# Kernel tuning notes

Hardware: AMD Instinct MI355X
Metric: run time of the kernel (lower is better)

## Reference

```python
import jax, jax.numpy as jnp
import numpy as np

ROUTING_ITERS = 3
EPS = 1e-12


def squash(s):
    # squash over both pose-matrix dims (axis=[-2,-1])
    n2 = jnp.sum(s * s, axis=(-2, -1), keepdims=True)
    n = jnp.sqrt(n2 + EPS)
    return s * (n2 / (1.0 + n2)) / n


def setup_inputs() -> dict:
    key = jax.random.key(0)
    k1, k2, k3 = jax.random.split(key, 3)
    B, I, O = 32, 4096, 32
    input_poses = jax.random.normal(k1, (B, I, 4, 4), dtype=jnp.float32)
    input_activations = jax.random.uniform(k2, (B, I), dtype=jnp.float32)
    # weight: [num_capsules, num_input_caps, 4, 4] (trans_in=trans_out=False for 4x4->4x4)
    w = jax.random.normal(k3, (O, I, 4, 4), dtype=jnp.float32) * 0.05
    return {"input_poses": input_poses, "input_activations": input_activations, "w": w}


def reference(input_poses, input_activations, w):
    # votes: expand_dims(poses,1) @ w, broadcast over output capsules -> [B,O,I,4,4]
    votes = jnp.einsum("bixy,oiyz->boixz", input_poses, w)
    B, O, I = votes.shape[0], votes.shape[1], votes.shape[2]

    # dynamic routing (routing-by-agreement)
    b = jnp.zeros((B, O, I), dtype=votes.dtype)
    s = None
    for it in range(ROUTING_ITERS):
        c = jax.nn.softmax(b, axis=1)  # couple over output capsules
        s = jnp.einsum("boi,boixy->boxy", c, votes)  # weighted sum [B,O,4,4]
        if it < ROUTING_ITERS - 1:
            v = squash(s)
            b = b + jnp.einsum("boixy,boxy->boi", votes, v)

    capsule_poses = squash(s)  # activation == 'squash'
    capsule_activations = jnp.sqrt(jnp.sum(capsule_poses * capsule_poses, axis=(-2, -1)) + EPS)
    return capsule_poses, capsule_activations
```

## Files before the change

### kernel.cpp

```cpp
#include <hip/hip_runtime.h>
#include <math.h>


#define NB 32
#define NI 4096
#define NO 32
#define I_TILE 16
#define NCHUNK (NI / I_TILE)
#define SOFF (NB * NO * 16)
#define EPSF 1e-12f

#define W_OSTR 10
#define W_ISTR (32 * W_OSTR)
#define W_WORDS (I_TILE * W_ISTR)
#define P_WORDS (NB * I_TILE * 8)

typedef _Float16 v2h __attribute__((ext_vector_type(2)));

#if __has_builtin(__builtin_amdgcn_fdot2)
__device__ __forceinline__ float fdot2(v2h a, v2h b, float c) {
    return __builtin_amdgcn_fdot2(a, b, c, false);
}
#else
__device__ __forceinline__ float fdot2(v2h a, v2h b, float c) {
    return fmaf((float)a.x, (float)b.x, fmaf((float)a.y, (float)b.y, c));
}
#endif

__device__ __forceinline__ v2h pk2h(float a, float b) {
    v2h r; r.x = (_Float16)a; r.y = (_Float16)b; return r;
}

__device__ __forceinline__ unsigned ubits(v2h x) {
    return __builtin_bit_cast(unsigned, x);
}

__device__ __forceinline__ v2h bch(unsigned u) {
    return __builtin_bit_cast(v2h, u);
}

__device__ __forceinline__ float dot4(const float4 a, const float4 b) {
    return fmaf(a.x, b.x, fmaf(a.y, b.y, fmaf(a.z, b.z, a.w * b.w)));
}

__device__ __forceinline__ void fma4(float4& s, const float c, const float4 t) {
    s.x = fmaf(c, t.x, s.x);
    s.y = fmaf(c, t.y, s.y);
    s.z = fmaf(c, t.z, s.z);
    s.w = fmaf(c, t.w, s.w);
}

template <int CTRL>
__device__ __forceinline__ float dpp_add(float x) {
    int xi = __builtin_bit_cast(int, x);
    int yi = __builtin_amdgcn_update_dpp(0, xi, CTRL, 0xf, 0xf, false);
    return x + __builtin_bit_cast(float, yi);
}

__device__ __forceinline__ float sum32(float x) {
    x = dpp_add<0xB1>(x);
    x = dpp_add<0x4E>(x);
    x = dpp_add<0x141>(x);
    x = dpp_add<0x140>(x);
#if __has_builtin(__builtin_amdgcn_permlane16_swap)
    typedef unsigned uv2 __attribute__((ext_vector_type(2)));
    const unsigned xi = __builtin_bit_cast(unsigned, x);
    uv2 r = __builtin_amdgcn_permlane16_swap(xi, xi, false, false);
    return __builtin_bit_cast(float, r.x) + __builtin_bit_cast(float, r.y);
#else
    int t = __builtin_amdgcn_ds_swizzle(__builtin_bit_cast(int, x), 0x401F);
    return x + __builtin_bit_cast(float, t);
#endif
}

__global__ __launch_bounds__(1024, 4) void caps_pass_w(
    const float* __restrict__ poses, const float* __restrict__ w,
    const float* __restrict__ v_buf, float* __restrict__ s_part,
    const int pass)
{
    __shared__ unsigned wsw[W_WORDS];
    __shared__ unsigned psw[P_WORDS];
    const int tid   = threadIdx.x;
    const int chunk = blockIdx.x;
    const int ibase = chunk * I_TILE;

    {
        const int o_l = tid >> 5;
        const int rem = tid & 31;
        const int i_l = rem >> 1;
        const int m   = rem & 1;
        const float* g = w + (((size_t)o_l * NI + ibase + i_l) << 4) + (m << 3);
        const float4 A = *(const float4*)g;
        const float4 B = *(const float4*)(g + 4);
        const int base = i_l * W_ISTR + o_l * W_OSTR + (m << 2);
        *(uint2*)&wsw[base]     = make_uint2(ubits(pk2h(A.x, B.x)),
                                             ubits(pk2h(A.y, B.y)));
        *(uint2*)&wsw[base + 2] = make_uint2(ubits(pk2h(A.z, B.z)),
                                             ubits(pk2h(A.w, B.w)));
    }
    {
        const int b_l = tid >> 5;
        const int rem = tid & 31;
        const int i_l = rem >> 1;
        const int x2  = rem & 1;
        const float* g = poses + (((size_t)b_l * NI + ibase + i_l) << 4)
                       + (x2 << 3);
        const float4 A = *(const float4*)g;
        const float4 B = *(const float4*)(g + 4);
        uint4 st;
        st.x = ubits(pk2h(A.x, A.y)); st.y = ubits(pk2h(A.z, A.w));
        st.z = ubits(pk2h(B.x, B.y)); st.w = ubits(pk2h(B.z, B.w));
        *(uint4*)&psw[((b_l * I_TILE + i_l) << 3) + (x2 << 2)] = st;
    }

    const int o    = tid & 31;
    const int bsub = tid >> 5;
    const int bo   = bsub * NO + o;

    float4 vv0 = {0,0,0,0}, vv1 = {0,0,0,0}, vv2 = {0,0,0,0}, vv3 = {0,0,0,0};
    if (pass > 0) {
        const float4* vp = (const float4*)(v_buf + (bo << 4));
        vv0 = vp[0]; vv1 = vp[1]; vv2 = vp[2]; vv3 = vp[3];
    }

    const unsigned* wrow = &wsw[o * W_OSTR];
    const unsigned* prow = &psw[(bsub * I_TILE) << 3];

    __syncthreads();

    float4 s0 = {0,0,0,0}, s1 = {0,0,0,0}, s2 = {0,0,0,0}, s3 = {0,0,0,0};

    #pragma unroll 2
    for (int i = 0; i < I_TILE; ++i) {
        const uint2 wa = *(const uint2*)&wrow[i * W_ISTR + 0];
        const uint2 wb = *(const uint2*)&wrow[i * W_ISTR + 2];
        const uint2 wc = *(const uint2*)&wrow[i * W_ISTR + 4];
        const uint2 wd = *(const uint2*)&wrow[i * W_ISTR + 6];
        const uint4 pa = *(const uint4*)&prow[(i << 3) + 0];
        const uint4 pb = *(const uint4*)&prow[(i << 3) + 4];

        const v2h p00 = bch(pa.x), p01 = bch(pa.y);
        const v2h p10 = bch(pa.z), p11 = bch(pa.w);
        const v2h p20 = bch(pb.x), p21 = bch(pb.y);
        const v2h p30 = bch(pb.z), p31 = bch(pb.w);
        const v2h w00 = bch(wa.x), w01 = bch(wa.y);
        const v2h w02 = bch(wb.x), w03 = bch(wb.y);
        const v2h w10 = bch(wc.x), w11 = bch(wc.y);
        const v2h w12 = bch(wd.x), w13 = bch(wd.y);

        float4 t0, t1, t2, t3;
        t0.x = fdot2(p00, w00, fdot2(p01, w10, 0.0f));
        t0.y = fdot2(p00, w01, fdot2(p01, w11, 0.0f));
        t0.z = fdot2(p00, w02, fdot2(p01, w12, 0.0f));
        t0.w = fdot2(p00, w03, fdot2(p01, w13, 0.0f));
        t1.x = fdot2(p10, w00, fdot2(p11, w10, 0.0f));
        t1.y = fdot2(p10, w01, fdot2(p11, w11, 0.0f));
        t1.z = fdot2(p10, w02, fdot2(p11, w12, 0.0f));
        t1.w = fdot2(p10, w03, fdot2(p11, w13, 0.0f));
        t2.x = fdot2(p20, w00, fdot2(p21, w10, 0.0f));
        t2.y = fdot2(p20, w01, fdot2(p21, w11, 0.0f));
        t2.z = fdot2(p20, w02, fdot2(p21, w12, 0.0f));
        t2.w = fdot2(p20, w03, fdot2(p21, w13, 0.0f));
        t3.x = fdot2(p30, w00, fdot2(p31, w10, 0.0f));
        t3.y = fdot2(p30, w01, fdot2(p31, w11, 0.0f));
        t3.z = fdot2(p30, w02, fdot2(p31, w12, 0.0f));
        t3.w = fdot2(p30, w03, fdot2(p31, w13, 0.0f));

        float cc;
        if (pass == 0) {
            cc = 1.0f / 32.0f;
        } else {
            const float d = dot4(t0,vv0) + dot4(t1,vv1)
                          + dot4(t2,vv2) + dot4(t3,vv3);
            const float e  = __expf(d);
            const float es = sum32(e);
            cc = __fdividef(e, es);
        }
        fma4(s0, cc, t0); fma4(s1, cc, t1);
        fma4(s2, cc, t2); fma4(s3, cc, t3);
    }

    float4* sp = (float4*)s_part;
    sp[(size_t)((chunk << 2) + 0) * (NB * NO) + bo] = s0;
    sp[(size_t)((chunk << 2) + 1) * (NB * NO) + bo] = s1;
    sp[(size_t)((chunk << 2) + 2) * (NB * NO) + bo] = s2;
    sp[(size_t)((chunk << 2) + 3) * (NB * NO) + bo] = s3;
}

__global__ __launch_bounds__(256) void caps_reduce(
    const float* __restrict__ s_part, float* __restrict__ v_buf,
    float* __restrict__ out, const int pass)
{
    const int e  = threadIdx.x & 63;
    const int c4 = threadIdx.x >> 6;
    const int eg = blockIdx.x * 64 + e;
    const int bo   = eg >> 4;
    const int k    = eg & 15;
    const int col  = ((k >> 2) << 12) + (bo << 2) + (k & 3);

    float acc = 0.0f;
    #pragma unroll 8
    for (int j = 0; j < NCHUNK / 4; ++j) {
        const int c = c4 * (NCHUNK / 4) + j;
        acc += s_part[(size_t)c * SOFF + col];
    }
    __shared__ float red[4][64];
    red[c4][e] = acc;
    __syncthreads();

    if (threadIdx.x < 64) {
        const float a = red[0][e] + red[1][e] + red[2][e] + red[3][e];
        float x = a * a;
        #pragma unroll
        for (int msk = 8; msk >= 1; msk >>= 1)
            x += __shfl_xor(x, msk, 16);
        const float n2 = x;
        const float n  = sqrtf(n2 + EPSF);
        const float sc = (n2 / (1.0f + n2)) / n;
        if (pass < 2) {
            const float vold = (pass == 0) ? 0.0f : v_buf[eg];
            v_buf[eg] = fmaf(sc, a, vold);
        } else {
            out[eg] = sc * a;
            if (k == 0)
                out[NB * NO * 16 + bo] = sqrtf(n2 * sc * sc + EPSF);
        }
    }
}

#define FB_CHUNKS 32
#define FB_IPB (NI / FB_CHUNKS)

__device__ __forceinline__ float4 row_mm(const float4 p, const float4 w0,
                                         const float4 w1, const float4 w2,
                                         const float4 w3) {
    float4 r;
    r.x = fmaf(p.x, w0.x, fmaf(p.y, w1.x, fmaf(p.z, w2.x, p.w * w3.x)));
    r.y = fmaf(p.x, w0.y, fmaf(p.y, w1.y, fmaf(p.z, w2.y, p.w * w3.y)));
    r.z = fmaf(p.x, w0.z, fmaf(p.y, w1.z, fmaf(p.z, w2.z, p.w * w3.z)));
    r.w = fmaf(p.x, w0.w, fmaf(p.y, w1.w, fmaf(p.z, w2.w, p.w * w3.w)));
    return r;
}

__global__ __launch_bounds__(256) void caps_pass_fb(
    const float* __restrict__ poses, const float* __restrict__ w,
    const float* __restrict__ v_buf, float* __restrict__ s_buf, const int mode)
{
    const int tid   = threadIdx.x;
    const int b     = blockIdx.y;
    const int chunk = blockIdx.x;
    const int o     = tid & 31;
    const int g     = tid >> 5;

    float4 v0 = {0,0,0,0}, v1 = {0,0,0,0}, v2 = {0,0,0,0}, v3 = {0,0,0,0};
    if (mode != 0) {
        const float4* vp = (const float4*)(v_buf + (((b * NO) + o) << 4));
        v0 = vp[0]; v1 = vp[1]; v2 = vp[2]; v3 = vp[3];
    }
    float4 s0 = {0,0,0,0}, s1 = {0,0,0,0}, s2 = {0,0,0,0}, s3 = {0,0,0,0};
    const int ibase = chunk * FB_IPB + g;
    #pragma unroll 4
    for (int it = 0; it < FB_IPB / 8; ++it) {
        const int i = ibase + (it << 3);
        const float4* ppf = (const float4*)(poses + ((((size_t)b * NI) + i) << 4));
        const float4 p0 = ppf[0], p1 = ppf[1], p2 = ppf[2], p3 = ppf[3];
        const float4* wpf = (const float4*)(w + ((((size_t)o * NI) + i) << 4));
        const float4 w0 = wpf[0], w1 = wpf[1], w2 = wpf[2], w3 = wpf[3];
        const float4 t0 = row_mm(p0, w0, w1, w2, w3);
        const float4 t1 = row_mm(p1, w0, w1, w2, w3);
        const float4 t2 = row_mm(p2, w0, w1, w2, w3);
        const float4 t3 = row_mm(p3, w0, w1, w2, w3);
        float cc;
        if (mode == 0) {
            cc = 1.0f / 32.0f;
        } else {
            float d = dot4(t0,v0) + dot4(t1,v1) + dot4(t2,v2) + dot4(t3,v3);
            const float e  = __expf(d);
            const float es = sum32(e);
            cc = __fdividef(e, es);
        }
        fma4(s0, cc, t0); fma4(s1, cc, t1);
        fma4(s2, cc, t2); fma4(s3, cc, t3);
    }
    __shared__ float red[8][32][16];
    float4* rp = (float4*)&red[g][o][0];
    rp[0] = s0; rp[1] = s1; rp[2] = s2; rp[3] = s3;
    __syncthreads();
    for (int idx = tid; idx < NO * 16; idx += 256) {
        const int oo = idx >> 4;
        const int kk = idx & 15;
        float acc = red[0][oo][kk];
        #pragma unroll
        for (int gg = 1; gg < 8; ++gg) acc += red[gg][oo][kk];
        atomicAdd(&s_buf[(((b * NO) + oo) << 4) + kk], acc);
    }
}

__global__ __launch_bounds__(256) void caps_squash_fb(
    float* __restrict__ s_buf, float* __restrict__ v_buf,
    float* __restrict__ out, const int mode)
{
    const int idx = blockIdx.x * 256 + threadIdx.x;
    if (idx >= NB * NO) return;
    float4* sp = (float4*)(s_buf + (idx << 4));
    const float4 s0 = sp[0], s1 = sp[1], s2 = sp[2], s3 = sp[3];
    const float n2 = dot4(s0,s0) + dot4(s1,s1) + dot4(s2,s2) + dot4(s3,s3);
    const float n  = sqrtf(n2 + EPSF);
    const float sc = (n2 / (1.0f + n2)) / n;
    if (mode == 2) {
        float4* op = (float4*)(out + (idx << 4));
        op[0] = make_float4(sc*s0.x, sc*s0.y, sc*s0.z, sc*s0.w);
        op[1] = make_float4(sc*s1.x, sc*s1.y, sc*s1.z, sc*s1.w);
        op[2] = make_float4(sc*s2.x, sc*s2.y, sc*s2.z, sc*s2.w);
        op[3] = make_float4(sc*s3.x, sc*s3.y, sc*s3.z, sc*s3.w);
        out[NB * NO * 16 + idx] = sqrtf(n2 * sc * sc + EPSF);
    } else {
        float4* vp = (float4*)(v_buf + (idx << 4));
        float4 a0 = {0,0,0,0}, a1 = {0,0,0,0}, a2 = {0,0,0,0}, a3 = {0,0,0,0};
        if (mode != 0) { a0 = vp[0]; a1 = vp[1]; a2 = vp[2]; a3 = vp[3]; }
        vp[0] = make_float4(fmaf(sc,s0.x,a0.x), fmaf(sc,s0.y,a0.y), fmaf(sc,s0.z,a0.z), fmaf(sc,s0.w,a0.w));
        vp[1] = make_float4(fmaf(sc,s1.x,a1.x), fmaf(sc,s1.y,a1.y), fmaf(sc,s1.z,a1.z), fmaf(sc,s1.w,a1.w));
        vp[2] = make_float4(fmaf(sc,s2.x,a2.x), fmaf(sc,s2.y,a2.y), fmaf(sc,s2.z,a2.z), fmaf(sc,s2.w,a2.w));
        vp[3] = make_float4(fmaf(sc,s3.x,a3.x), fmaf(sc,s3.y,a3.y), fmaf(sc,s3.z,a3.z), fmaf(sc,s3.w,a3.w));
        const float4 z = {0,0,0,0};
        sp[0] = z; sp[1] = z; sp[2] = z; sp[3] = z;
    }
}

extern "C" void kernel_launch(void* const* d_in, const int* in_sizes, int n_in,
                              void* d_out, int out_size, void* d_ws, size_t ws_size,
                              hipStream_t stream) {
    const float* poses = (const float*)d_in[0];
    const float* w     = (const float*)d_in[2];
    float* out = (float*)d_out;

    const size_t need = ((size_t)NCHUNK * SOFF + SOFF) * sizeof(float);
    if (ws_size >= need) {
        float* s_part = (float*)d_ws;
        float* v_buf  = s_part + (size_t)NCHUNK * SOFF;
        dim3 gp(NCHUNK), blkp(1024), gr(256), blkr(256);
        for (int pass = 0; pass < 3; ++pass) {
            caps_pass_w<<<gp, blkp, 0, stream>>>(poses, w, v_buf, s_part, pass);
            caps_reduce<<<gr, blkr, 0, stream>>>(s_part, v_buf, out, pass);
        }
    } else {
        float* s_buf = (float*)d_ws;
        float* v_buf = s_buf + SOFF;
        (void)hipMemsetAsync(s_buf, 0, SOFF * sizeof(float), stream);
        dim3 grid(FB_CHUNKS, NB), block(256);
        for (int pass = 0; pass < 3; ++pass) {
            caps_pass_fb<<<grid, block, 0, stream>>>(poses, w, v_buf, s_buf, pass);
            caps_squash_fb<<<4, 256, 0, stream>>>(s_buf, v_buf, out, pass);
        }
    }
}
```

Before: 136.7 us.

## Fuse routing passes into one cooperative kernel with grid syncs

New measurement: 364.4 us. 166% more time.

```diff
diff --git a/kernel.cpp b/kernel.cpp
--- a/kernel.cpp
+++ b/kernel.cpp
@@ -1,5 +1,8 @@
 #include <hip/hip_runtime.h>
+#include <hip/hip_cooperative_groups.h>
 #include <math.h>
+
+namespace cg = cooperative_groups;
 
 
 #define NB 32
@@ -73,44 +76,42 @@
 #endif
 }
 
-__global__ __launch_bounds__(1024, 4) void caps_pass_w(
-    const float* __restrict__ poses, const float* __restrict__ w,
-    const float* __restrict__ v_buf, float* __restrict__ s_part,
-    const int pass)
-{
-    __shared__ unsigned wsw[W_WORDS];
-    __shared__ unsigned psw[P_WORDS];
-    const int tid   = threadIdx.x;
-    const int chunk = blockIdx.x;
+__device__ __forceinline__ void pass_body(
+    unsigned* wsw, unsigned* psw,
+    const float* poses, const float* w,
+    const float* v_buf, float* s_part,
+    const int chunk, const int tid, const int pass, const bool do_stage)
+{
     const int ibase = chunk * I_TILE;
-
-    {
-        const int o_l = tid >> 5;
-        const int rem = tid & 31;
-        const int i_l = rem >> 1;
-        const int m   = rem & 1;
-        const float* g = w + (((size_t)o_l * NI + ibase + i_l) << 4) + (m << 3);
-        const float4 A = *(const float4*)g;
-        const float4 B = *(const float4*)(g + 4);
-        const int base = i_l * W_ISTR + o_l * W_OSTR + (m << 2);
-        *(uint2*)&wsw[base]     = make_uint2(ubits(pk2h(A.x, B.x)),
-                                             ubits(pk2h(A.y, B.y)));
-        *(uint2*)&wsw[base + 2] = make_uint2(ubits(pk2h(A.z, B.z)),
-                                             ubits(pk2h(A.w, B.w)));
-    }
-    {
-        const int b_l = tid >> 5;
-        const int rem = tid & 31;
-        const int i_l = rem >> 1;
-        const int x2  = rem & 1;
-        const float* g = poses + (((size_t)b_l * NI + ibase + i_l) << 4)
-                       + (x2 << 3);
-        const float4 A = *(const float4*)g;
-        const float4 B = *(const float4*)(g + 4);
-        uint4 st;
-        st.x = ubits(pk2h(A.x, A.y)); st.y = ubits(pk2h(A.z, A.w));
-        st.z = ubits(pk2h(B.x, B.y)); st.w = ubits(pk2h(B.z, B.w));
-        *(uint4*)&psw[((b_l * I_TILE + i_l) << 3) + (x2 << 2)] = st;
+    if (do_stage) {
+        {
+            const int o_l = tid >> 5;
+            const int rem = tid & 31;
+            const int i_l = rem >> 1;
+            const int m   = rem & 1;
+            const float* g = w + (((size_t)o_l * NI + ibase + i_l) << 4) + (m << 3);
+            const float4 A = *(const float4*)g;
+            const float4 B = *(const float4*)(g + 4);
+            const int base = i_l * W_ISTR + o_l * W_OSTR + (m << 2);
+            *(uint2*)&wsw[base]     = make_uint2(ubits(pk2h(A.x, B.x)),
+                                                 ubits(pk2h(A.y, B.y)));
+            *(uint2*)&wsw[base + 2] = make_uint2(ubits(pk2h(A.z, B.z)),
+                                                 ubits(pk2h(A.w, B.w)));
+        }
+        {
+            const int b_l = tid >> 5;
+            const int rem = tid & 31;
+            const int i_l = rem >> 1;
+            const int x2  = rem & 1;
+            const float* g = poses + (((size_t)b_l * NI + ibase + i_l) << 4)
+                           + (x2 << 3);
+            const float4 A = *(const float4*)g;
+            const float4 B = *(const float4*)(g + 4);
+            uint4 st;
+            st.x = ubits(pk2h(A.x, A.y)); st.y = ubits(pk2h(A.z, A.w));
+            st.z = ubits(pk2h(B.x, B.y)); st.w = ubits(pk2h(B.z, B.w));
+            *(uint4*)&psw[((b_l * I_TILE + i_l) << 3) + (x2 << 2)] = st;
+        }
     }
 
     const int o    = tid & 31;
@@ -187,144 +188,69 @@
     sp[(size_t)((chunk << 2) + 3) * (NB * NO) + bo] = s3;
 }
 
-__global__ __launch_bounds__(256) void caps_reduce(
+__device__ __forceinline__ void reduce_body(
+    const float* s_part, float* v_buf, float* out, const int eg, const int pass)
+{
+    const int bo  = eg >> 4;
+    const int k   = eg & 15;
+    const int col = ((k >> 2) << 12) + (bo << 2) + (k & 3);
+    float acc = 0.0f;
+    #pragma unroll 8
+    for (int c = 0; c < NCHUNK; ++c)
+        acc += s_part[(size_t)c * SOFF + col];
+    float x = acc * acc;
+    #pragma unroll
+    for (int msk = 8; msk >= 1; msk >>= 1)
+        x += __shfl_xor(x, msk, 16);
+    const float n2 = x;
+    const float n  = sqrtf(n2 + EPSF);
+    const float sc = (n2 / (1.0f + n2)) / n;
+    if (pass < 2) {
+        const float vold = (pass == 0) ? 0.0f : v_buf[eg];
+        v_buf[eg] = fmaf(sc, acc, vold);
+    } else {
+        out[eg] = sc * acc;
+        if (k == 0)
+            out[NB * NO * 16 + bo] = sqrtf(n2 * sc * sc + EPSF);
+    }
+}
+
+__global__ __launch_bounds__(1024) void caps_coop(
+    const float* __restrict__ poses, const float* __restrict__ w,
+    float* __restrict__ s_part, float* __restrict__ v_buf,
+    float* __restrict__ out)
+{
+    __shared__ unsigned wsw[W_WORDS];
+    __shared__ unsigned psw[P_WORDS];
+    cg::grid_group grid = cg::this_grid();
+    const int tid = threadIdx.x;
+    const int blk = blockIdx.x;
+
+    for (int pass = 0; pass < 3; ++pass) {
+        pass_body(wsw, psw, poses, w, v_buf, s_part, blk, tid, pass, pass == 0);
+        grid.sync();
+        if (blk < 16)
+            reduce_body(s_part, v_buf, out, (blk << 10) + tid, pass);
+        if (pass < 2) grid.sync();
+    }
+}
+
+__global__ __launch_bounds__(1024) void caps_pass_sep(
+    const float* __restrict__ poses, const float* __restrict__ w,
+    const float* __restrict__ v_buf, float* __restrict__ s_part,
+    const int pass)
+{
+    __shared__ unsigned wsw[W_WORDS];
+    __shared__ unsigned psw[P_WORDS];
+    pass_body(wsw, psw, poses, w, v_buf, s_part,
+              blockIdx.x, threadIdx.x, pass, true);
+}
+
+__global__ __launch_bounds__(1024) void caps_reduce_sep(
     const float* __restrict__ s_part, float* __restrict__ v_buf,
     float* __restrict__ out, const int pass)
 {
-    const int e  = threadIdx.x & 63;
-    const int c4 = threadIdx.x >> 6;
-    const int eg = blockIdx.x * 64 + e;
-    const int bo   = eg >> 4;
-    const int k    = eg & 15;
-    const int col  = ((k >> 2) << 12) + (bo << 2) + (k & 3);
-
-    float acc = 0.0f;
-    #pragma unroll 8
-    for (int j = 0; j < NCHUNK / 4; ++j) {
-        const int c = c4 * (NCHUNK / 4) + j;
-        acc += s_part[(size_t)c * SOFF + col];
-    }
-    __shared__ float red[4][64];
-    red[c4][e] = acc;
-    __syncthreads();
-
-    if (threadIdx.x < 64) {
-        const float a = red[0][e] + red[1][e] + red[2][e] + red[3][e];
-        float x = a * a;
-        #pragma unroll
-        for (int msk = 8; msk >= 1; msk >>= 1)
-            x += __shfl_xor(x, msk, 16);
-        const float n2 = x;
-        const float n  = sqrtf(n2 + EPSF);
-        const float sc = (n2 / (1.0f + n2)) / n;
-        if (pass < 2) {
-            const float vold = (pass == 0) ? 0.0f : v_buf[eg];
-            v_buf[eg] = fmaf(sc, a, vold);
-        } else {
-            out[eg] = sc * a;
-            if (k == 0)
-                out[NB * NO * 16 + bo] = sqrtf(n2 * sc * sc + EPSF);
-        }
-    }
-}
-
-#define FB_CHUNKS 32
-#define FB_IPB (NI / FB_CHUNKS)
-
-__device__ __forceinline__ float4 row_mm(const float4 p, const float4 w0,
-                                         const float4 w1, const float4 w2,
-                                         const float4 w3) {
-    float4 r;
-    r.x = fmaf(p.x, w0.x, fmaf(p.y, w1.x, fmaf(p.z, w2.x, p.w * w3.x)));
-    r.y = fmaf(p.x, w0.y, fmaf(p.y, w1.y, fmaf(p.z, w2.y, p.w * w3.y)));
-    r.z = fmaf(p.x, w0.z, fmaf(p.y, w1.z, fmaf(p.z, w2.z, p.w * w3.z)));
-    r.w = fmaf(p.x, w0.w, fmaf(p.y, w1.w, fmaf(p.z, w2.w, p.w * w3.w)));
-    return r;
-}
-
-__global__ __launch_bounds__(256) void caps_pass_fb(
-    const float* __restrict__ poses, const float* __restrict__ w,
-    const float* __restrict__ v_buf, float* __restrict__ s_buf, const int mode)
-{
-    const int tid   = threadIdx.x;
-    const int b     = blockIdx.y;
-    const int chunk = blockIdx.x;
-    const int o     = tid & 31;
-    const int g     = tid >> 5;
-
-    float4 v0 = {0,0,0,0}, v1 = {0,0,0,0}, v2 = {0,0,0,0}, v3 = {0,0,0,0};
-    if (mode != 0) {
-        const float4* vp = (const float4*)(v_buf + (((b * NO) + o) << 4));
-        v0 = vp[0]; v1 = vp[1]; v2 = vp[2]; v3 = vp[3];
-    }
-    float4 s0 = {0,0,0,0}, s1 = {0,0,0,0}, s2 = {0,0,0,0}, s3 = {0,0,0,0};
-    const int ibase = chunk * FB_IPB + g;
-    #pragma unroll 4
-    for (int it = 0; it < FB_IPB / 8; ++it) {
-        const int i = ibase + (it << 3);
-        const float4* ppf = (const float4*)(poses + ((((size_t)b * NI) + i) << 4));
-        const float4 p0 = ppf[0], p1 = ppf[1], p2 = ppf[2], p3 = ppf[3];
-        const float4* wpf = (const float4*)(w + ((((size_t)o * NI) + i) << 4));
-        const float4 w0 = wpf[0], w1 = wpf[1], w2 = wpf[2], w3 = wpf[3];
-        const float4 t0 = row_mm(p0, w0, w1, w2, w3);
-        const float4 t1 = row_mm(p1, w0, w1, w2, w3);
-        const float4 t2 = row_mm(p2, w0, w1, w2, w3);
-        const float4 t3 = row_mm(p3, w0, w1, w2, w3);
-        float cc;
-        if (mode == 0) {
-            cc = 1.0f / 32.0f;
-        } else {
-            float d = dot4(t0,v0) + dot4(t1,v1) + dot4(t2,v2) + dot4(t3,v3);
-            const float e  = __expf(d);
-            const float es = sum32(e);
-            cc = __fdividef(e, es);
-        }
-        fma4(s0, cc, t0); fma4(s1, cc, t1);
-        fma4(s2, cc, t2); fma4(s3, cc, t3);
-    }
-    __shared__ float red[8][32][16];
-    float4* rp = (float4*)&red[g][o][0];
-    rp[0] = s0; rp[1] = s1; rp[2] = s2; rp[3] = s3;
-    __syncthreads();
-    for (int idx = tid; idx < NO * 16; idx += 256) {
-        const int oo = idx >> 4;
-        const int kk = idx & 15;
-        float acc = red[0][oo][kk];
-        #pragma unroll
-        for (int gg = 1; gg < 8; ++gg) acc += red[gg][oo][kk];
-        atomicAdd(&s_buf[(((b * NO) + oo) << 4) + kk], acc);
-    }
-}
-
-__global__ __launch_bounds__(256) void caps_squash_fb(
-    float* __restrict__ s_buf, float* __restrict__ v_buf,
-    float* __restrict__ out, const int mode)
-{
-    const int idx = blockIdx.x * 256 + threadIdx.x;
-    if (idx >= NB * NO) return;
-    float4* sp = (float4*)(s_buf + (idx << 4));
-    const float4 s0 = sp[0], s1 = sp[1], s2 = sp[2], s3 = sp[3];
-    const float n2 = dot4(s0,s0) + dot4(s1,s1) + dot4(s2,s2) + dot4(s3,s3);
-    const float n  = sqrtf(n2 + EPSF);
-    const float sc = (n2 / (1.0f + n2)) / n;
-    if (mode == 2) {
-        float4* op = (float4*)(out + (idx << 4));
-        op[0] = make_float4(sc*s0.x, sc*s0.y, sc*s0.z, sc*s0.w);
-        op[1] = make_float4(sc*s1.x, sc*s1.y, sc*s1.z, sc*s1.w);
-        op[2] = make_float4(sc*s2.x, sc*s2.y, sc*s2.z, sc*s2.w);
-        op[3] = make_float4(sc*s3.x, sc*s3.y, sc*s3.z, sc*s3.w);
-        out[NB * NO * 16 + idx] = sqrtf(n2 * sc * sc + EPSF);
-    } else {
-        float4* vp = (float4*)(v_buf + (idx << 4));
-        float4 a0 = {0,0,0,0}, a1 = {0,0,0,0}, a2 = {0,0,0,0}, a3 = {0,0,0,0};
-        if (mode != 0) { a0 = vp[0]; a1 = vp[1]; a2 = vp[2]; a3 = vp[3]; }
-        vp[0] = make_float4(fmaf(sc,s0.x,a0.x), fmaf(sc,s0.y,a0.y), fmaf(sc,s0.z,a0.z), fmaf(sc,s0.w,a0.w));
-        vp[1] = make_float4(fmaf(sc,s1.x,a1.x), fmaf(sc,s1.y,a1.y), fmaf(sc,s1.z,a1.z), fmaf(sc,s1.w,a1.w));
-        vp[2] = make_float4(fmaf(sc,s2.x,a2.x), fmaf(sc,s2.y,a2.y), fmaf(sc,s2.z,a2.z), fmaf(sc,s2.w,a2.w));
-        vp[3] = make_float4(fmaf(sc,s3.x,a3.x), fmaf(sc,s3.y,a3.y), fmaf(sc,s3.z,a3.z), fmaf(sc,s3.w,a3.w));
-        const float4 z = {0,0,0,0};
-        sp[0] = z; sp[1] = z; sp[2] = z; sp[3] = z;
-    }
+    reduce_body(s_part, v_buf, out, (blockIdx.x << 10) + threadIdx.x, pass);
 }
 
 extern "C" void kernel_launch(void* const* d_in, const int* in_sizes, int n_in,
@@ -332,25 +258,24 @@
                               hipStream_t stream) {
     const float* poses = (const float*)d_in[0];
     const float* w     = (const float*)d_in[2];
-    float* out = (float*)d_out;
-
-    const size_t need = ((size_t)NCHUNK * SOFF + SOFF) * sizeof(float);
-    if (ws_size >= need) {
-        float* s_part = (float*)d_ws;
-        float* v_buf  = s_part + (size_t)NCHUNK * SOFF;
-        dim3 gp(NCHUNK), blkp(1024), gr(256), blkr(256);
+    float* out   = (float*)d_out;
+    float* s_part = (float*)d_ws;
+    float* v_buf  = s_part + (size_t)NCHUNK * SOFF;
+
+    void* args[5];
+    args[0] = (void*)&poses;
+    args[1] = (void*)&w;
+    args[2] = (void*)&s_part;
+    args[3] = (void*)&v_buf;
+    args[4] = (void*)&out;
+    hipError_t err = hipLaunchCooperativeKernel(
+        (void*)caps_coop, dim3(NCHUNK), dim3(1024), args, 0, stream);
+
+    if (err != hipSuccess) {
         for (int pass = 0; pass < 3; ++pass) {
-            caps_pass_w<<<gp, blkp, 0, stream>>>(poses, w, v_buf, s_part, pass);
-            caps_reduce<<<gr, blkr, 0, stream>>>(s_part, v_buf, out, pass);
-        }
-    } else {
-        float* s_buf = (float*)d_ws;
-        float* v_buf = s_buf + SOFF;
-        (void)hipMemsetAsync(s_buf, 0, SOFF * sizeof(float), stream);
-        dim3 grid(FB_CHUNKS, NB), block(256);
-        for (int pass = 0; pass < 3; ++pass) {
-            caps_pass_fb<<<grid, block, 0, stream>>>(poses, w, v_buf, s_buf, pass);
-            caps_squash_fb<<<4, 256, 0, stream>>>(s_buf, v_buf, out, pass);
-        }
-    }
-}
+            caps_pass_sep<<<NCHUNK, 1024, 0, stream>>>(poses, w, v_buf,
+                                                       s_part, pass);
+            caps_reduce_sep<<<16, 1024, 0, stream>>>(s_part, v_buf, out, pass);
+        }
+    }
+}
```
